# Kernel optimization log

Measured on AMD Instinct MI355X. Metric: run time of the kernel, lower is better.

## Reference

```python
import jax, jax.numpy as jnp
import numpy as np

V, D, H, FF, L, ER_LEN = 267, 512, 8, 1024, 6, 2048
HD = D // H
NEG = -1e9


def sinusoidal_pe(S, d, dtype):
    pos = np.arange(S)[:, None].astype(np.float32)
    div = np.exp(np.arange(0, d, 2).astype(np.float32) * (-np.log(10000.0) / d))
    pe = np.zeros((S, d), dtype=np.float32)
    pe[:, 0::2] = np.sin(pos * div)
    pe[:, 1::2] = np.cos(pos * div)
    return jnp.asarray(pe, dtype=dtype)[:, None, :]  # [S,1,D]


def layernorm(x, g, b, eps=1e-5):
    mu = jnp.mean(x, -1, keepdims=True)
    var = jnp.var(x, -1, keepdims=True)
    return (x - mu) * jax.lax.rsqrt(var + eps) * g + b


def skew(qe):
    # qe: [B,H,S,S] -> Music-Transformer skew producing srel [B,H,S,S]
    S = qe.shape[-1]
    mask = jnp.flip(jnp.triu(jnp.ones((S, S), qe.dtype)), axis=0)
    qe = qe * mask
    qe = jnp.pad(qe, ((0, 0), (0, 0), (0, 0), (1, 0)))
    qe = qe.reshape(qe.shape[0], qe.shape[1], S + 1, S)
    return qe[:, :, 1:, :]


def setup_inputs() -> dict:
    key = jax.random.key(0)
    ks = jax.random.split(key, 20)
    s = 0.02
    inp = {
        'inputs_seq': jax.random.randint(ks[0], (2, 2048), 0, V),
        'emb': jax.random.normal(ks[1], (V, D)) * s,
        'in_proj_w': jax.random.normal(ks[2], (L, 3 * D, D)) * s,
        'in_proj_b': jnp.zeros((L, 3 * D)),
        'out_proj_w': jax.random.normal(ks[3], (L, D, D)) * s,
        'out_proj_b': jnp.zeros((L, D)),
        'er': jax.random.normal(ks[4], (L, ER_LEN, HD)) * s,
        'lin1_w': jax.random.normal(ks[5], (L, FF, D)) * s,
        'lin1_b': jnp.zeros((L, FF)),
        'lin2_w': jax.random.normal(ks[6], (L, D, FF)) * s,
        'lin2_b': jnp.zeros((L, D)),
        'ln1_g': jnp.ones((L, D)), 'ln1_b': jnp.zeros((L, D)),
        'ln2_g': jnp.ones((L, D)), 'ln2_b': jnp.zeros((L, D)),
        'fln_g': jnp.ones((D,)), 'fln_b': jnp.zeros((D,)),
        'wout_w': jax.random.normal(ks[7], (V, D)) * s,
        'wout_b': jnp.zeros((V,)),
    }
    return inp


def reference(inputs_seq, emb, in_proj_w, in_proj_b, out_proj_w, out_proj_b, er,
              lin1_w, lin1_b, lin2_w, lin2_b, ln1_g, ln1_b, ln2_g, ln2_b,
              fln_g, fln_b, wout_w, wout_b):
    B, S = inputs_seq.shape
    x = emb[inputs_seq]                       # [B,S,D]
    x = jnp.transpose(x, (1, 0, 2))           # [S,B,D] seq-first
    x = x + sinusoidal_pe(S, D, x.dtype)
    causal = jnp.triu(jnp.full((S, S), NEG, x.dtype), k=1)
    er_start = max(0, ER_LEN - S)
    scale = 1.0 / jnp.sqrt(jnp.asarray(HD, x.dtype))

    for i in range(L):
        qkv = jnp.einsum('sbd,ed->sbe', x, in_proj_w[i]) + in_proj_b[i]
        q, k, v = jnp.split(qkv, 3, axis=-1)
        # [S,B,D] -> [B,H,S,hd]
        def heads(t):
            return jnp.transpose(t.reshape(S, B, H, HD), (1, 2, 0, 3))
        q, k, v = heads(q) * scale, heads(k), heads(v)
        scores = jnp.einsum('bhqd,bhkd->bhqk', q, k)
        qe = jnp.einsum('bhqd,ed->bhqe', q, er[i][er_start:])
        scores = scores + skew(qe) + causal
        attn = jax.nn.softmax(scores, axis=-1)
        ctx = jnp.einsum('bhqk,bhkd->bhqd', attn, v)
        ctx = jnp.transpose(ctx, (2, 0, 1, 3)).reshape(S, B, D)
        attn_out = jnp.einsum('sbd,ed->sbe', ctx, out_proj_w[i]) + out_proj_b[i]
        x = layernorm(x + attn_out, ln1_g[i], ln1_b[i])
        h = jax.nn.relu(jnp.einsum('sbd,fd->sbf', x, lin1_w[i]) + lin1_b[i])
        ff = jnp.einsum('sbf,df->sbd', h, lin2_w[i]) + lin2_b[i]
        x = layernorm(x + ff, ln2_g[i], ln2_b[i])

    x = layernorm(x, fln_g, fln_b)
    return jnp.einsum('sbd,vd->sbv', x, wout_w) + wout_b  # [S,B,V]
```

## Files before the change

kernel.cpp:

```cpp
#include <hip/hip_runtime.h>
#include <hip/hip_bf16.h>

typedef __attribute__((ext_vector_type(4))) float f32x4;
typedef __attribute__((ext_vector_type(8))) short bf16x8;
typedef __attribute__((ext_vector_type(2))) unsigned short u16x2;
typedef __attribute__((ext_vector_type(4))) unsigned short u16x4;
typedef __attribute__((ext_vector_type(8))) unsigned short u16x8;

#define S_LEN 2048
#define BATCH 2
#define DMODEL 512
#define NHEAD 8
#define HDIM 64
#define MROWS 4096
#define LAYERS 6

#define MFMA16(a, b, c) __builtin_amdgcn_mfma_f32_16x16x32_bf16((a), (b), (c), 0, 0, 0)

__device__ __forceinline__ float bf2f(unsigned short u) {
    return __uint_as_float(((unsigned)u) << 16);
}
__device__ __forceinline__ unsigned short f2bf(float f) {
    union { float f; unsigned u; } v; v.f = f;
    unsigned r = v.u + 0x7FFF + ((v.u >> 16) & 1);
    return (unsigned short)(r >> 16);
}
__device__ __forceinline__ bf16x8 load8(const unsigned short* p) {
    return *reinterpret_cast<const bf16x8*>(p);
}

__global__ __launch_bounds__(256) void f2bf_kernel(
    const float* __restrict__ src, unsigned short* __restrict__ dst, int n8)
{
    int i = blockIdx.x * 256 + threadIdx.x;
    if (i >= n8) return;
    f32x4 a = *reinterpret_cast<const f32x4*>(src + (size_t)i * 8);
    f32x4 b = *reinterpret_cast<const f32x4*>(src + (size_t)i * 8 + 4);
    u16x8 o;
#pragma unroll
    for (int j = 0; j < 4; ++j) { o[j] = f2bf(a[j]); o[4 + j] = f2bf(b[j]); }
    *reinterpret_cast<u16x8*>(dst + (size_t)i * 8) = o;
}

__global__ __launch_bounds__(256) void embed_pe_kernel(
    const int* __restrict__ seq, const float* __restrict__ emb,
    float* __restrict__ x, unsigned short* __restrict__ x16)
{
    const int r = blockIdx.x;
    const int j = threadIdx.x;
    const int s = r >> 1, b = r & 1;
    const int tok = seq[b * S_LEN + s];
    const float e0 = emb[(size_t)tok * DMODEL + 2 * j];
    const float e1 = emb[(size_t)tok * DMODEL + 2 * j + 1];
    const double c = -9.210340371976184 / 512.0;
    double dv = exp((double)(2 * j) * c);
    double arg = (double)s * dv;
    const float v0 = e0 + (float)sin(arg);
    const float v1 = e1 + (float)cos(arg);
    x[(size_t)r * DMODEL + 2 * j]     = v0;
    x[(size_t)r * DMODEL + 2 * j + 1] = v1;
    u16x2 o; o[0] = f2bf(v0); o[1] = f2bf(v1);
    *reinterpret_cast<u16x2*>(x16 + (size_t)r * DMODEL + 2 * j) = o;
}

template<int BM>
__global__ __launch_bounds__(256) void gemm_mfma_kernel(
    const unsigned short* __restrict__ A, const unsigned short* __restrict__ W,
    const float* __restrict__ bias,
    float* __restrict__ Cf, unsigned short* __restrict__ Cb,
    int N, int K, int relu, int qscale)
{
    constexpr int MF = BM / 32;
    __shared__ __align__(16) unsigned short As[BM * 64];
    __shared__ __align__(16) unsigned short Bs[64 * 64];
    const int tid = threadIdx.x;
    const int w = tid >> 6, lane = tid & 63, l15 = lane & 15, hi = lane >> 4;
    const int wm = w >> 1, wn = w & 1;
    const int n0 = blockIdx.x * 64, m0 = blockIdx.y * BM;
    const int sr = tid >> 3;
    const int ss = tid & 7;

    bf16x8 aprf[MF], bprf[2];
    auto loadA = [&](int k0) {
#pragma unroll
        for (int i = 0; i < MF; ++i) {
            const int r = sr + 32 * i;
            aprf[i] = load8(A + (size_t)(m0 + r) * K + k0 + ((ss ^ ((r >> 1) & 7)) * 8));
        }
    };
    auto loadB = [&](int k0) {
#pragma unroll
        for (int i = 0; i < 2; ++i) {
            const int r = sr + 32 * i;
            const int nn = n0 + r;
            if (nn < N) bprf[i] = load8(W + (size_t)nn * K + k0 + ((ss ^ ((r >> 1) & 7)) * 8));
            else { u16x8 z = {0,0,0,0,0,0,0,0}; bprf[i] = *reinterpret_cast<bf16x8*>(&z); }
        }
    };

    f32x4 acc[MF][2];
#pragma unroll
    for (int mf = 0; mf < MF; ++mf)
#pragma unroll
        for (int nf = 0; nf < 2; ++nf) acc[mf][nf] = f32x4{0.f, 0.f, 0.f, 0.f};

    loadA(0); loadB(0);
    for (int k0 = 0; k0 < K; k0 += 64) {
        __syncthreads();
#pragma unroll
        for (int i = 0; i < MF; ++i)
            *reinterpret_cast<bf16x8*>(As + (sr + 32 * i) * 64 + ss * 8) = aprf[i];
#pragma unroll
        for (int i = 0; i < 2; ++i)
            *reinterpret_cast<bf16x8*>(Bs + (sr + 32 * i) * 64 + ss * 8) = bprf[i];
        if (k0 + 64 < K) { loadA(k0 + 64); loadB(k0 + 64); }
        __syncthreads();

        bf16x8 af[MF][2], bfr[2][2];
#pragma unroll
        for (int mf = 0; mf < MF; ++mf) {
            const int r = wm * (BM / 2) + mf * 16 + l15;
            const int sw = (r >> 1) & 7;
            const unsigned short* base = As + r * 64;
            af[mf][0] = *reinterpret_cast<const bf16x8*>(base + ((hi ^ sw) * 8));
            af[mf][1] = *reinterpret_cast<const bf16x8*>(base + (((hi + 4) ^ sw) * 8));
        }
#pragma unroll
        for (int nf = 0; nf < 2; ++nf) {
            const int r = wn * 32 + nf * 16 + l15;
            const int sw = (r >> 1) & 7;
            const unsigned short* base = Bs + r * 64;
            bfr[nf][0] = *reinterpret_cast<const bf16x8*>(base + ((hi ^ sw) * 8));
            bfr[nf][1] = *reinterpret_cast<const bf16x8*>(base + (((hi + 4) ^ sw) * 8));
        }
#pragma unroll
        for (int mf = 0; mf < MF; ++mf)
#pragma unroll
            for (int nf = 0; nf < 2; ++nf) {
                acc[mf][nf] = MFMA16(af[mf][0], bfr[nf][0], acc[mf][nf]);
                acc[mf][nf] = MFMA16(af[mf][1], bfr[nf][1], acc[mf][nf]);
            }
    }

#pragma unroll
    for (int nf = 0; nf < 2; ++nf) {
        const int col = n0 + wn * 32 + nf * 16 + l15;
        const bool okc = col < N;
        const float bv = okc ? bias[col] : 0.f;
        const float sc = (qscale && col < 512) ? 0.125f : 1.f;
#pragma unroll
        for (int mf = 0; mf < MF; ++mf) {
            const int rbase = m0 + wm * (BM / 2) + mf * 16 + hi * 4;
#pragma unroll
            for (int rg = 0; rg < 4; ++rg) {
                float v = acc[mf][nf][rg] + bv;
                if (relu) v = fmaxf(v, 0.f);
                v *= sc;
                if (okc) {
                    const size_t idx = (size_t)(rbase + rg) * N + col;
                    if (Cb) Cb[idx] = f2bf(v);
                    else    Cf[idx] = v;
                }
            }
        }
    }
}

__global__ __launch_bounds__(256, 2) void attn_mfma_kernel(
    const unsigned short* __restrict__ qkv16, const unsigned short* __restrict__ er16,
    unsigned short* __restrict__ part16, float* __restrict__ mlbuf)
{
    __shared__ __align__(16) unsigned short K_s[64 * 64];
    __shared__ __align__(16) unsigned short V_T[64 * 64];
    __shared__ __align__(16) unsigned short Er_s[64 * 64];
    __shared__ __align__(16) unsigned short E_w[4 * 16 * 196];

    const int tid  = threadIdx.x;
    const int w    = tid >> 6;
    const int lane = tid & 63;
    const int l15  = lane & 15;
    const int hi   = lane >> 4;
    const int bx   = blockIdx.y;
    const int bh   = blockIdx.x;
    const int b    = bh >> 3, hh = bh & 7;
    const int sk   = lane;
    const int dg0  = w;

    int qb, c;
    if (bx < 32) { qb = 31 - (bx >> 1); c = bx & 1; }
    else         { qb = 15 - (bx - 32); c = 0; }
    const int pidx = bh * 48 + bx;
    const int q0   = qb * 64;
    const int k0s  = c * 1024;
    const int ntl  = min(qb + 1 - c * 16, 16);
    const int qg   = q0 + 16 * w + l15;

    const unsigned short* qptr = qkv16 + ((size_t)qg * BATCH + b) * 1536 + hh * HDIM;
    bf16x8 qf0 = load8(qptr + hi * 8);
    bf16x8 qf1 = load8(qptr + 32 + hi * 8);

    unsigned short* ewp = E_w + (w * 16 + l15) * 196;
    const int E0  = 1984 - q0 + k0s;
    const int E0m = E0 % 192;

#pragma unroll 2
    for (int mf = 0; mf < 8; ++mf) {
        int e = E0 + mf * 16 + l15;
        int ec = e > 2047 ? 2047 : e;
        bf16x8 a0 = load8(er16 + (size_t)ec * 64 + hi * 8);
        bf16x8 a1 = load8(er16 + (size_t)ec * 64 + 32 + hi * 8);
        f32x4 acc = {0.f, 0.f, 0.f, 0.f};
        acc = MFMA16(a0, qf0, acc);
        acc = MFMA16(a1, qf1, acc);
        int col = E0m + mf * 16 + 4 * hi;
        if (col >= 192) col -= 192;
        u16x4 ew;
#pragma unroll
        for (int r = 0; r < 4; ++r) ew[r] = f2bf(acc[r]);
        *reinterpret_cast<u16x4*>(ewp + col) = ew;
    }

    float m = -INFINITY, lsum = 0.f;
    f32x4 acc_o[4];
#pragma unroll
    for (int mf = 0; mf < 4; ++mf) acc_o[mf] = f32x4{0.f, 0.f, 0.f, 0.f};

    int col0t = (2047 - qg + k0s) % 192;

    bf16x8 kpr0, kpr1, vpr0, vpr1, epr0, epr1;
    {
        const unsigned short* krow = qkv16 + ((size_t)(k0s + sk) * BATCH + b) * 1536 + 512 + hh * HDIM;
        kpr0 = load8(krow + dg0 * 8);       kpr1 = load8(krow + (dg0 + 4) * 8);
        vpr0 = load8(krow + 512 + dg0 * 8); vpr1 = load8(krow + 512 + (dg0 + 4) * 8);
    }
    if (ntl > 1) {
        int e = E0 + 128 + sk;
        int ec = e > 2047 ? 2047 : e;
        epr0 = load8(er16 + (size_t)ec * 64 + dg0 * 8);
        epr1 = load8(er16 + (size_t)ec * 64 + (dg0 + 4) * 8);
    }

    for (int t = 0; t < ntl; ++t) {
        const int k0 = k0s + t * 64;
        const bool doE = (t + 1 < ntl);
        __syncthreads();
        *reinterpret_cast<bf16x8*>(K_s + sk * 64 + ((dg0 ^ (sk & 7)) * 8)) = kpr0;
        *reinterpret_cast<bf16x8*>(K_s + sk * 64 + (((dg0 + 4) ^ (sk & 7)) * 8)) = kpr1;
#pragma unroll
        for (int jj = 0; jj < 8; ++jj) {
            const int d0 = dg0 * 8 + jj;
            const int d1 = (dg0 + 4) * 8 + jj;
            V_T[d0 * 64 + (((sk >> 3) ^ (d0 & 7)) * 8) + (sk & 7)] = (unsigned short)vpr0[jj];
            V_T[d1 * 64 + (((sk >> 3) ^ (d1 & 7)) * 8) + (sk & 7)] = (unsigned short)vpr1[jj];
        }
        if (doE) {
            *reinterpret_cast<bf16x8*>(Er_s + sk * 64 + ((dg0 ^ (sk & 7)) * 8)) = epr0;
            *reinterpret_cast<bf16x8*>(Er_s + sk * 64 + (((dg0 + 4) ^ (sk & 7)) * 8)) = epr1;
        }
        if (t + 1 < ntl) {
            const unsigned short* krow = qkv16 + ((size_t)(k0 + 64 + sk) * BATCH + b) * 1536 + 512 + hh * HDIM;
            kpr0 = load8(krow + dg0 * 8);       kpr1 = load8(krow + (dg0 + 4) * 8);
            vpr0 = load8(krow + 512 + dg0 * 8); vpr1 = load8(krow + 512 + (dg0 + 4) * 8);
            if (t + 2 < ntl) {
                int e = E0 + 128 + 64 * (t + 1) + sk;
                int ec = e > 2047 ? 2047 : e;
                epr0 = load8(er16 + (size_t)ec * 64 + dg0 * 8);
                epr1 = load8(er16 + (size_t)ec * 64 + (dg0 + 4) * 8);
            }
        }
        __syncthreads();

        f32x4 sacc[4];
#pragma unroll
        for (int f = 0; f < 4; ++f) {
            const int row = l15 + 16 * f;
            bf16x8 ka0 = *reinterpret_cast<const bf16x8*>(K_s + row * 64 + (((0 + hi) ^ (l15 & 7)) * 8));
            bf16x8 ka1 = *reinterpret_cast<const bf16x8*>(K_s + row * 64 + (((4 + hi) ^ (l15 & 7)) * 8));
            f32x4 z = {0.f, 0.f, 0.f, 0.f};
            z = MFMA16(ka0, qf0, z);
            sacc[f] = MFMA16(ka1, qf1, z);
        }

        if (doE) {
            const int fbm = (E0 + 128 + 64 * t) % 192;
#pragma unroll
            for (int mf = 0; mf < 4; ++mf) {
                const int rr = l15 + 16 * mf;
                bf16x8 a0 = *reinterpret_cast<const bf16x8*>(Er_s + rr * 64 + ((hi ^ (l15 & 7)) * 8));
                bf16x8 a1 = *reinterpret_cast<const bf16x8*>(Er_s + rr * 64 + (((hi + 4) ^ (l15 & 7)) * 8));
                f32x4 acc = {0.f, 0.f, 0.f, 0.f};
                acc = MFMA16(a0, qf0, acc);
                acc = MFMA16(a1, qf1, acc);
                int col = fbm + mf * 16 + 4 * hi;
                u16x4 ew;
#pragma unroll
                for (int r = 0; r < 4; ++r) ew[r] = f2bf(acc[r]);
                *reinterpret_cast<u16x4*>(ewp + col) = ew;
            }
        }

        float mt = -INFINITY;
#pragma unroll
        for (int f = 0; f < 4; ++f) {
#pragma unroll
            for (int r = 0; r < 4; ++r) {
                const int kk = 16 * f + 4 * hi + r;
                int col = col0t + kk;
                if (col >= 192) col -= 192;
                float sv = sacc[f][r] + bf2f(ewp[col]);
                if (k0 + kk > qg) sv = -1e9f;
                sacc[f][r] = sv;
                mt = fmaxf(mt, sv);
            }
        }
        mt = fmaxf(mt, __shfl_xor(mt, 16));
        mt = fmaxf(mt, __shfl_xor(mt, 32));
        const float mn = fmaxf(m, mt);
        const float corr = __expf(m - mn);
        float ps = 0.f;
#pragma unroll
        for (int f = 0; f < 4; ++f)
#pragma unroll
            for (int r = 0; r < 4; ++r) {
                const float e = __expf(sacc[f][r] - mn);
                sacc[f][r] = e; ps += e;
            }
        ps += __shfl_xor(ps, 16);
        ps += __shfl_xor(ps, 32);
        lsum = lsum * corr + ps;
        m = mn;

        bf16x8 pf0, pf1;
#pragma unroll
        for (int j = 0; j < 8; ++j) {
            pf0[j] = (short)f2bf(sacc[j >> 2][j & 3]);
            pf1[j] = (short)f2bf(sacc[(j >> 2) + 2][j & 3]);
        }

#pragma unroll
        for (int mf = 0; mf < 4; ++mf) {
            f32x4 a = acc_o[mf];
            a[0] *= corr; a[1] *= corr; a[2] *= corr; a[3] *= corr;
            const unsigned short* vrow = V_T + (l15 + 16 * mf) * 64;
            const int sw = l15 & 7;
#pragma unroll
            for (int kh = 0; kh < 2; ++kh) {
                u16x4 va = *reinterpret_cast<const u16x4*>(vrow + ((((hi >> 1) + 4 * kh) ^ sw) * 8) + 4 * (hi & 1));
                u16x4 vb = *reinterpret_cast<const u16x4*>(vrow + ((((hi >> 1) + 2 + 4 * kh) ^ sw) * 8) + 4 * (hi & 1));
                bf16x8 vf;
#pragma unroll
                for (int j = 0; j < 4; ++j) { vf[j] = (short)va[j]; vf[4 + j] = (short)vb[j]; }
                a = MFMA16(vf, kh ? pf1 : pf0, a);
            }
            acc_o[mf] = a;
        }

        col0t += 64;
        if (col0t >= 192) col0t -= 192;
    }

    unsigned short* pa = part16 + ((size_t)pidx * 64 + 16 * w + l15) * 64;
#pragma unroll
    for (int mf = 0; mf < 4; ++mf) {
        u16x4 o;
#pragma unroll
        for (int r = 0; r < 4; ++r) o[r] = f2bf(acc_o[mf][r]);
        *reinterpret_cast<u16x4*>(pa + 16 * mf + 4 * hi) = o;
    }
    if (hi == 0) {
        float* ml = mlbuf + ((size_t)pidx * 64 + 16 * w + l15) * 2;
        ml[0] = m; ml[1] = lsum;
    }
}

__global__ __launch_bounds__(256) void attn_combine_kernel(
    const unsigned short* __restrict__ part16, const float* __restrict__ mlbuf,
    unsigned short* __restrict__ ctx16)
{
    const int flat = blockIdx.x * 256 + threadIdx.x;
    const int qi = flat >> 3, dg = flat & 7;
    const int bh = qi >> 11, ql = qi & 2047;
    const int b = bh >> 3, hh = bh & 7;
    const int qb = ql >> 6, rl = ql & 63;

    float o[8];
    u16x8 res;
    if (qb >= 16) {
        const int i0 = bh * 48 + 2 * (31 - qb);
        const int i1 = i0 + 1;
        u16x8 a0 = *reinterpret_cast<const u16x8*>(part16 + ((size_t)i0 * 64 + rl) * 64 + dg * 8);
        u16x8 a1 = *reinterpret_cast<const u16x8*>(part16 + ((size_t)i1 * 64 + rl) * 64 + dg * 8);
        const float* ml0 = mlbuf + ((size_t)i0 * 64 + rl) * 2;
        const float* ml1 = mlbuf + ((size_t)i1 * 64 + rl) * 2;
        const float m0 = ml0[0], l0 = ml0[1], m1 = ml1[0], l1 = ml1[1];
        const float ms = fmaxf(m0, m1);
        const float w0 = __expf(m0 - ms), w1 = __expf(m1 - ms);
        const float inv = 1.f / (l0 * w0 + l1 * w1);
#pragma unroll
        for (int j = 0; j < 8; ++j)
            o[j] = (bf2f(a0[j]) * w0 + bf2f(a1[j]) * w1) * inv;
    } else {
        const int i0 = bh * 48 + 32 + (15 - qb);
        u16x8 a0 = *reinterpret_cast<const u16x8*>(part16 + ((size_t)i0 * 64 + rl) * 64 + dg * 8);
        const float inv = 1.f / mlbuf[((size_t)i0 * 64 + rl) * 2 + 1];
#pragma unroll
        for (int j = 0; j < 8; ++j) o[j] = bf2f(a0[j]) * inv;
    }
#pragma unroll
    for (int j = 0; j < 8; ++j) res[j] = f2bf(o[j]);
    *reinterpret_cast<u16x8*>(ctx16 + ((size_t)ql * BATCH + b) * DMODEL + hh * HDIM + dg * 8) = res;
}

__global__ __launch_bounds__(256) void ln_kernel(
    const float* __restrict__ xin, const float* __restrict__ res,
    const float* __restrict__ gg, const float* __restrict__ bb,
    float* __restrict__ xout, unsigned short* __restrict__ x16out, int has_res)
{
    const int w = threadIdx.x >> 6, lane = threadIdx.x & 63;
    const int row = blockIdx.x * 4 + w;
    const float* xp = xin + (size_t)row * DMODEL + lane * 8;
    f32x4 v0 = *reinterpret_cast<const f32x4*>(xp);
    f32x4 v1 = *reinterpret_cast<const f32x4*>(xp + 4);
    if (has_res) {
        const float* rp = res + (size_t)row * DMODEL + lane * 8;
        v0 += *reinterpret_cast<const f32x4*>(rp);
        v1 += *reinterpret_cast<const f32x4*>(rp + 4);
    }
    float sum = 0.f, ssq = 0.f;
#pragma unroll
    for (int c2 = 0; c2 < 4; ++c2) {
        sum += v0[c2] + v1[c2];
        ssq += v0[c2] * v0[c2] + v1[c2] * v1[c2];
    }
#pragma unroll
    for (int off = 32; off > 0; off >>= 1) {
        sum += __shfl_xor(sum, off);
        ssq += __shfl_xor(ssq, off);
    }
    const float mu = sum * (1.f / 512.f);
    const float var = ssq * (1.f / 512.f) - mu * mu;
    const float rstd = rsqrtf(var + 1e-5f);
    f32x4 g0 = *reinterpret_cast<const f32x4*>(gg + lane * 8);
    f32x4 g1 = *reinterpret_cast<const f32x4*>(gg + lane * 8 + 4);
    f32x4 b0 = *reinterpret_cast<const f32x4*>(bb + lane * 8);
    f32x4 b1 = *reinterpret_cast<const f32x4*>(bb + lane * 8 + 4);
    f32x4 o0, o1;
    u16x8 h;
#pragma unroll
    for (int c2 = 0; c2 < 4; ++c2) {
        o0[c2] = (v0[c2] - mu) * rstd * g0[c2] + b0[c2];
        o1[c2] = (v1[c2] - mu) * rstd * g1[c2] + b1[c2];
        h[c2] = f2bf(o0[c2]); h[4 + c2] = f2bf(o1[c2]);
    }
    float* op = xout + (size_t)row * DMODEL + lane * 8;
    *reinterpret_cast<f32x4*>(op)     = o0;
    *reinterpret_cast<f32x4*>(op + 4) = o1;
    *reinterpret_cast<u16x8*>(x16out + (size_t)row * DMODEL + lane * 8) = h;
}

extern "C" void kernel_launch(void* const* d_in, const int* in_sizes, int n_in,
                              void* d_out, int out_size, void* d_ws, size_t ws_size,
                              hipStream_t stream)
{
    const int*   seq  = (const int*)d_in[0];
    const float* emb  = (const float*)d_in[1];
    const float* ipw  = (const float*)d_in[2];
    const float* ipb  = (const float*)d_in[3];
    const float* opw  = (const float*)d_in[4];
    const float* opb  = (const float*)d_in[5];
    const float* er   = (const float*)d_in[6];
    const float* l1w  = (const float*)d_in[7];
    const float* l1b  = (const float*)d_in[8];
    const float* l2w  = (const float*)d_in[9];
    const float* l2b  = (const float*)d_in[10];
    const float* ln1g = (const float*)d_in[11];
    const float* ln1b = (const float*)d_in[12];
    const float* ln2g = (const float*)d_in[13];
    const float* ln2b = (const float*)d_in[14];
    const float* flng = (const float*)d_in[15];
    const float* flnb = (const float*)d_in[16];
    const float* ww   = (const float*)d_in[17];
    const float* wb   = (const float*)d_in[18];
    float* out = (float*)d_out;

    float* xf  = (float*)d_ws;
    float* tmp = xf + (size_t)MROWS * DMODEL;
    unsigned short* x16   = (unsigned short*)(tmp + (size_t)MROWS * DMODEL);
    unsigned short* qkv16 = x16   + (size_t)MROWS * DMODEL;
    unsigned short* ctx16 = qkv16 + (size_t)MROWS * 1536;
    unsigned short* er16  = ctx16 + (size_t)MROWS * DMODEL;
    unsigned short* w16   = er16  + (size_t)LAYERS * S_LEN * HDIM;
    unsigned short* h16   = qkv16;
    unsigned short* part16 = (unsigned short*)tmp;
    float* mlbuf = (float*)(part16 + (size_t)768 * 64 * 64);

    unsigned short* ipw16 = w16;
    unsigned short* opw16 = ipw16 + (size_t)LAYERS * 1536 * DMODEL;
    unsigned short* l1w16 = opw16 + (size_t)LAYERS * DMODEL * DMODEL;
    unsigned short* l2w16 = l1w16 + (size_t)LAYERS * 1024 * DMODEL;
    unsigned short* ww16  = l2w16 + (size_t)LAYERS * DMODEL * 1024;

    {
        int n8;
        n8 = LAYERS * 1536 * DMODEL / 8; f2bf_kernel<<<(n8 + 255) / 256, 256, 0, stream>>>(ipw, ipw16, n8);
        n8 = LAYERS * DMODEL * DMODEL / 8; f2bf_kernel<<<(n8 + 255) / 256, 256, 0, stream>>>(opw, opw16, n8);
        n8 = LAYERS * 1024 * DMODEL / 8; f2bf_kernel<<<(n8 + 255) / 256, 256, 0, stream>>>(l1w, l1w16, n8);
        n8 = LAYERS * DMODEL * 1024 / 8; f2bf_kernel<<<(n8 + 255) / 256, 256, 0, stream>>>(l2w, l2w16, n8);
        n8 = 267 * DMODEL / 8;           f2bf_kernel<<<(n8 + 255) / 256, 256, 0, stream>>>(ww, ww16, n8);
        n8 = LAYERS * S_LEN * HDIM / 8;  f2bf_kernel<<<(n8 + 255) / 256, 256, 0, stream>>>(er, er16, n8);
    }

    embed_pe_kernel<<<MROWS, 256, 0, stream>>>(seq, emb, xf, x16);

    for (int i = 0; i < LAYERS; ++i) {
        gemm_mfma_kernel<128><<<dim3(24, 32), 256, 0, stream>>>(
            x16, ipw16 + (size_t)i * 1536 * DMODEL, ipb + (size_t)i * 1536,
            nullptr, qkv16, 1536, DMODEL, 0, 1);
        attn_mfma_kernel<<<dim3(BATCH * NHEAD, 48), 256, 0, stream>>>(
            qkv16, er16 + (size_t)i * S_LEN * HDIM, part16, mlbuf);
        attn_combine_kernel<<<1024, 256, 0, stream>>>(part16, mlbuf, ctx16);
        gemm_mfma_kernel<64><<<dim3(8, 64), 256, 0, stream>>>(
            ctx16, opw16 + (size_t)i * DMODEL * DMODEL, opb + (size_t)i * DMODEL,
            tmp, nullptr, DMODEL, DMODEL, 0, 0);
        ln_kernel<<<MROWS / 4, 256, 0, stream>>>(
            xf, tmp, ln1g + (size_t)i * DMODEL, ln1b + (size_t)i * DMODEL, xf, x16, 1);
        gemm_mfma_kernel<128><<<dim3(16, 32), 256, 0, stream>>>(
            x16, l1w16 + (size_t)i * 1024 * DMODEL, l1b + (size_t)i * 1024,
            nullptr, h16, 1024, DMODEL, 1, 0);
        gemm_mfma_kernel<64><<<dim3(8, 64), 256, 0, stream>>>(
            h16, l2w16 + (size_t)i * DMODEL * 1024, l2b + (size_t)i * DMODEL,
            tmp, nullptr, DMODEL, 1024, 0, 0);
        ln_kernel<<<MROWS / 4, 256, 0, stream>>>(
            xf, tmp, ln2g + (size_t)i * DMODEL, ln2b + (size_t)i * DMODEL, xf, x16, 1);
    }

    ln_kernel<<<MROWS / 4, 256, 0, stream>>>(xf, nullptr, flng, flnb, xf, x16, 0);
    gemm_mfma_kernel<64><<<dim3(5, 64), 256, 0, stream>>>(
        x16, ww16, wb, out, nullptr, 267, DMODEL, 0, 0);
}
```

Baseline: 807.7 us.

## Write V pre-transposed from QKV GEMM epilogue to simplify attention V staging

The QKV projection GEMM now writes Q and K into a narrower 1024-wide buffer and scatters V into a per-head, per-tile transposed layout whose key positions are permuted to match the MFMA operand order. The attention kernel can then stage V into shared memory with two 16-byte vector stores instead of sixteen scalar transposing stores, and read its PV operands as whole 8-element vectors rather than assembling them from 4-element pieces. The cost moves into the GEMM epilogue, which now performs scattered 2-byte global writes for the V third of its output.

```diff
diff --git a/kernel.cpp b/kernel.cpp
--- a/kernel.cpp
+++ b/kernel.cpp
@@ -68,7 +68,8 @@
     const unsigned short* __restrict__ A, const unsigned short* __restrict__ W,
     const float* __restrict__ bias,
     float* __restrict__ Cf, unsigned short* __restrict__ Cb,
-    int N, int K, int relu, int qscale)
+    unsigned short* __restrict__ vT,
+    int N, int K, int relu, int qkvsplit)
 {
     constexpr int MF = BM / 32;
     __shared__ __align__(16) unsigned short As[BM * 64];
@@ -147,7 +148,6 @@
         const int col = n0 + wn * 32 + nf * 16 + l15;
         const bool okc = col < N;
         const float bv = okc ? bias[col] : 0.f;
-        const float sc = (qscale && col < 512) ? 0.125f : 1.f;
 #pragma unroll
         for (int mf = 0; mf < MF; ++mf) {
             const int rbase = m0 + wm * (BM / 2) + mf * 16 + hi * 4;
@@ -155,11 +155,25 @@
             for (int rg = 0; rg < 4; ++rg) {
                 float v = acc[mf][nf][rg] + bv;
                 if (relu) v = fmaxf(v, 0.f);
-                v *= sc;
                 if (okc) {
-                    const size_t idx = (size_t)(rbase + rg) * N + col;
-                    if (Cb) Cb[idx] = f2bf(v);
-                    else    Cf[idx] = v;
+                    const int row = rbase + rg;
+                    if (qkvsplit) {
+                        if (col < 1024) {
+                            if (col < 512) v *= 0.125f;
+                            Cb[(size_t)row * 1024 + col] = f2bf(v);
+                        } else {
+                            const int h = (col - 1024) >> 6, d = (col - 1024) & 63;
+                            const int s = row >> 1, bb = row & 1;
+                            const int kt = s >> 6, kin = s & 63;
+                            const int pos = (kin & 3) | (((kin >> 4) & 1) << 2)
+                                          | (((kin >> 2) & 3) << 3) | (kin & 32);
+                            vT[((((size_t)(bb * 8 + h) * 32 + kt) * 64 + d) << 6) + pos] = f2bf(v);
+                        }
+                    } else {
+                        const size_t idx = (size_t)row * N + col;
+                        if (Cb) Cb[idx] = f2bf(v);
+                        else    Cf[idx] = v;
+                    }
                 }
             }
         }
@@ -167,7 +181,8 @@
 }
 
 __global__ __launch_bounds__(256, 2) void attn_mfma_kernel(
-    const unsigned short* __restrict__ qkv16, const unsigned short* __restrict__ er16,
+    const unsigned short* __restrict__ qk16, const unsigned short* __restrict__ vT16,
+    const unsigned short* __restrict__ er16,
     unsigned short* __restrict__ part16, float* __restrict__ mlbuf)
 {
     __shared__ __align__(16) unsigned short K_s[64 * 64];
@@ -185,6 +200,8 @@
     const int b    = bh >> 3, hh = bh & 7;
     const int sk   = lane;
     const int dg0  = w;
+    const int dv0  = 16 * w + (lane >> 3);
+    const int gv   = lane & 7;
 
     int qb, c;
     if (bx < 32) { qb = 31 - (bx >> 1); c = bx & 1; }
@@ -195,7 +212,7 @@
     const int ntl  = min(qb + 1 - c * 16, 16);
     const int qg   = q0 + 16 * w + l15;
 
-    const unsigned short* qptr = qkv16 + ((size_t)qg * BATCH + b) * 1536 + hh * HDIM;
+    const unsigned short* qptr = qk16 + ((size_t)qg * BATCH + b) * 1024 + hh * HDIM;
     bf16x8 qf0 = load8(qptr + hi * 8);
     bf16x8 qf1 = load8(qptr + 32 + hi * 8);
 
@@ -229,9 +246,11 @@
 
     bf16x8 kpr0, kpr1, vpr0, vpr1, epr0, epr1;
     {
-        const unsigned short* krow = qkv16 + ((size_t)(k0s + sk) * BATCH + b) * 1536 + 512 + hh * HDIM;
+        const unsigned short* krow = qk16 + ((size_t)(k0s + sk) * BATCH + b) * 1024 + 512 + hh * HDIM;
         kpr0 = load8(krow + dg0 * 8);       kpr1 = load8(krow + (dg0 + 4) * 8);
-        vpr0 = load8(krow + 512 + dg0 * 8); vpr1 = load8(krow + 512 + (dg0 + 4) * 8);
+        const unsigned short* vbase = vT16 + (((size_t)bh * 32 + (k0s >> 6)) * 64) * 64;
+        vpr0 = load8(vbase + dv0 * 64 + gv * 8);
+        vpr1 = load8(vbase + (dv0 + 8) * 64 + gv * 8);
     }
     if (ntl > 1) {
         int e = E0 + 128 + sk;
@@ -246,21 +265,18 @@
         __syncthreads();
         *reinterpret_cast<bf16x8*>(K_s + sk * 64 + ((dg0 ^ (sk & 7)) * 8)) = kpr0;
         *reinterpret_cast<bf16x8*>(K_s + sk * 64 + (((dg0 + 4) ^ (sk & 7)) * 8)) = kpr1;
-#pragma unroll
-        for (int jj = 0; jj < 8; ++jj) {
-            const int d0 = dg0 * 8 + jj;
-            const int d1 = (dg0 + 4) * 8 + jj;
-            V_T[d0 * 64 + (((sk >> 3) ^ (d0 & 7)) * 8) + (sk & 7)] = (unsigned short)vpr0[jj];
-            V_T[d1 * 64 + (((sk >> 3) ^ (d1 & 7)) * 8) + (sk & 7)] = (unsigned short)vpr1[jj];
-        }
+        *reinterpret_cast<bf16x8*>(V_T + dv0 * 64 + ((gv ^ (dv0 & 7)) * 8)) = vpr0;
+        *reinterpret_cast<bf16x8*>(V_T + (dv0 + 8) * 64 + ((gv ^ (dv0 & 7)) * 8)) = vpr1;
         if (doE) {
             *reinterpret_cast<bf16x8*>(Er_s + sk * 64 + ((dg0 ^ (sk & 7)) * 8)) = epr0;
             *reinterpret_cast<bf16x8*>(Er_s + sk * 64 + (((dg0 + 4) ^ (sk & 7)) * 8)) = epr1;
         }
         if (t + 1 < ntl) {
-            const unsigned short* krow = qkv16 + ((size_t)(k0 + 64 + sk) * BATCH + b) * 1536 + 512 + hh * HDIM;
+            const unsigned short* krow = qk16 + ((size_t)(k0 + 64 + sk) * BATCH + b) * 1024 + 512 + hh * HDIM;
             kpr0 = load8(krow + dg0 * 8);       kpr1 = load8(krow + (dg0 + 4) * 8);
-            vpr0 = load8(krow + 512 + dg0 * 8); vpr1 = load8(krow + 512 + (dg0 + 4) * 8);
+            const unsigned short* vbase = vT16 + (((size_t)bh * 32 + ((k0 + 64) >> 6)) * 64) * 64;
+            vpr0 = load8(vbase + dv0 * 64 + gv * 8);
+            vpr1 = load8(vbase + (dv0 + 8) * 64 + gv * 8);
             if (t + 2 < ntl) {
                 int e = E0 + 128 + 64 * (t + 1) + sk;
                 int ec = e > 2047 ? 2047 : e;
@@ -343,15 +359,10 @@
             a[0] *= corr; a[1] *= corr; a[2] *= corr; a[3] *= corr;
             const unsigned short* vrow = V_T + (l15 + 16 * mf) * 64;
             const int sw = l15 & 7;
-#pragma unroll
-            for (int kh = 0; kh < 2; ++kh) {
-                u16x4 va = *reinterpret_cast<const u16x4*>(vrow + ((((hi >> 1) + 4 * kh) ^ sw) * 8) + 4 * (hi & 1));
-                u16x4 vb = *reinterpret_cast<const u16x4*>(vrow + ((((hi >> 1) + 2 + 4 * kh) ^ sw) * 8) + 4 * (hi & 1));
-                bf16x8 vf;
-#pragma unroll
-                for (int j = 0; j < 4; ++j) { vf[j] = (short)va[j]; vf[4 + j] = (short)vb[j]; }
-                a = MFMA16(vf, kh ? pf1 : pf0, a);
-            }
+            bf16x8 vf0 = *reinterpret_cast<const bf16x8*>(vrow + ((hi ^ sw) * 8));
+            bf16x8 vf1 = *reinterpret_cast<const bf16x8*>(vrow + (((4 + hi) ^ sw) * 8));
+            a = MFMA16(vf0, pf0, a);
+            a = MFMA16(vf1, pf1, a);
             acc_o[mf] = a;
         }
 
@@ -486,11 +497,12 @@
     float* xf  = (float*)d_ws;
     float* tmp = xf + (size_t)MROWS * DMODEL;
     unsigned short* x16   = (unsigned short*)(tmp + (size_t)MROWS * DMODEL);
-    unsigned short* qkv16 = x16   + (size_t)MROWS * DMODEL;
-    unsigned short* ctx16 = qkv16 + (size_t)MROWS * 1536;
+    unsigned short* qk16  = x16  + (size_t)MROWS * DMODEL;
+    unsigned short* ctx16 = qk16 + (size_t)MROWS * 1024;
     unsigned short* er16  = ctx16 + (size_t)MROWS * DMODEL;
-    unsigned short* w16   = er16  + (size_t)LAYERS * S_LEN * HDIM;
-    unsigned short* h16   = qkv16;
+    unsigned short* vT16  = er16 + (size_t)LAYERS * S_LEN * HDIM;
+    unsigned short* w16   = vT16 + (size_t)16 * 32 * 64 * 64;
+    unsigned short* h16   = qk16;
     unsigned short* part16 = (unsigned short*)tmp;
     float* mlbuf = (float*)(part16 + (size_t)768 * 64 * 64);
 
@@ -515,26 +527,26 @@
     for (int i = 0; i < LAYERS; ++i) {
         gemm_mfma_kernel<128><<<dim3(24, 32), 256, 0, stream>>>(
             x16, ipw16 + (size_t)i * 1536 * DMODEL, ipb + (size_t)i * 1536,
-            nullptr, qkv16, 1536, DMODEL, 0, 1);
+            nullptr, qk16, vT16, 1536, DMODEL, 0, 1);
         attn_mfma_kernel<<<dim3(BATCH * NHEAD, 48), 256, 0, stream>>>(
-            qkv16, er16 + (size_t)i * S_LEN * HDIM, part16, mlbuf);
+            qk16, vT16, er16 + (size_t)i * S_LEN * HDIM, part16, mlbuf);
         attn_combine_kernel<<<1024, 256, 0, stream>>>(part16, mlbuf, ctx16);
         gemm_mfma_kernel<64><<<dim3(8, 64), 256, 0, stream>>>(
             ctx16, opw16 + (size_t)i * DMODEL * DMODEL, opb + (size_t)i * DMODEL,
-            tmp, nullptr, DMODEL, DMODEL, 0, 0);
+            tmp, nullptr, nullptr, DMODEL, DMODEL, 0, 0);
         ln_kernel<<<MROWS / 4, 256, 0, stream>>>(
             xf, tmp, ln1g + (size_t)i * DMODEL, ln1b + (size_t)i * DMODEL, xf, x16, 1);
         gemm_mfma_kernel<128><<<dim3(16, 32), 256, 0, stream>>>(
             x16, l1w16 + (size_t)i * 1024 * DMODEL, l1b + (size_t)i * 1024,
-            nullptr, h16, 1024, DMODEL, 1, 0);
+            nullptr, h16, nullptr, 1024, DMODEL, 1, 0);
         gemm_mfma_kernel<64><<<dim3(8, 64), 256, 0, stream>>>(
             h16, l2w16 + (size_t)i * DMODEL * 1024, l2b + (size_t)i * DMODEL,
-            tmp, nullptr, DMODEL, 1024, 0, 0);
+            tmp, nullptr, nullptr, DMODEL, 1024, 0, 0);
         ln_kernel<<<MROWS / 4, 256, 0, stream>>>(
             xf, tmp, ln2g + (size_t)i * DMODEL, ln2b + (size_t)i * DMODEL, xf, x16, 1);
     }
 
     ln_kernel<<<MROWS / 4, 256, 0, stream>>>(xf, nullptr, flng, flnb, xf, x16, 0);
     gemm_mfma_kernel<64><<<dim3(5, 64), 256, 0, stream>>>(
-        x16, ww16, wb, out, nullptr, 267, DMODEL, 0, 0);
-}
+        x16, ww16, wb, out, nullptr, nullptr, 267, DMODEL, 0, 0);
+}
```

Result: faster. 770.7 us (-4.6%).
